# Optimization experiments

Hardware: AMD Instinct MI355X
Metric: run time of the kernel (lower is better)

Reference implementation:

```python
import jax, jax.numpy as jnp
import numpy as np

OVERLAP_THRESHOLD = 0.5
NEG_POS_RATIO = 3
ALPHA = 1.0


def cxcy_to_xy(cxcy):
    return jnp.concatenate([cxcy[..., :2] - cxcy[..., 2:] / 2,
                            cxcy[..., :2] + cxcy[..., 2:] / 2], axis=-1)


def xy_to_cxcy(xy):
    return jnp.concatenate([(xy[..., :2] + xy[..., 2:]) / 2,
                            xy[..., 2:] - xy[..., :2]], axis=-1)


def cxcy_to_gcxgcy(cxcy, priors_cxcy):
    return jnp.concatenate([
        (cxcy[..., :2] - priors_cxcy[..., :2]) / (priors_cxcy[..., 2:] / 10.0),
        jnp.log(cxcy[..., 2:] / priors_cxcy[..., 2:]) * 5.0], axis=-1)


def jaccard(a, b):
    # a: [N,4] xy, b: [P,4] xy -> [N,P]
    lo = jnp.maximum(a[:, None, :2], b[None, :, :2])
    hi = jnp.minimum(a[:, None, 2:], b[None, :, 2:])
    inter = jnp.prod(jnp.clip(hi - lo, 0.0), axis=-1)  # [N,P]
    area_a = jnp.prod(a[:, 2:] - a[:, :2], axis=-1)  # [N]
    area_b = jnp.prod(b[:, 2:] - b[:, :2], axis=-1)  # [P]
    return inter / (area_a[:, None] + area_b[None, :] - inter)


def _match_one(boxes_i, labels_i, priors_cxcy, priors_xy):
    n_objects = boxes_i.shape[0]
    overlap = jaccard(boxes_i, priors_xy)  # [N,P]
    overlap_for_each_prior = overlap.max(axis=0)  # [P]
    object_for_each_prior = overlap.argmax(axis=0)  # [P]
    prior_for_each_object = overlap.argmax(axis=1)  # [N]
    # force each object to own its best prior
    object_for_each_prior = object_for_each_prior.at[prior_for_each_object].set(
        jnp.arange(n_objects))
    overlap_for_each_prior = overlap_for_each_prior.at[prior_for_each_object].set(1.0)
    labels_for_each_prior = labels_i[object_for_each_prior]
    labels_for_each_prior = jnp.where(overlap_for_each_prior < OVERLAP_THRESHOLD,
                                      0, labels_for_each_prior)
    matched = boxes_i[object_for_each_prior]  # [P,4]
    true_locs = cxcy_to_gcxgcy(xy_to_cxcy(matched), priors_cxcy)  # [P,4]
    return true_locs, labels_for_each_prior


def reference(predicted_locs, predicted_scores, boxes, labels, priors_cxcy):
    B, P, C = predicted_scores.shape
    priors_xy = cxcy_to_xy(priors_cxcy)
    true_locs, true_classes = jax.vmap(
        _match_one, in_axes=(0, 0, None, None))(boxes, labels, priors_cxcy, priors_xy)
    # true_locs: [B,P,4], true_classes: [B,P]
    positive = true_classes != 0  # [B,P]
    n_pos = positive.sum(axis=1)  # [B]
    n_pos_total = n_pos.sum()

    # SmoothL1 (beta=1, mean over selected elements = n_pos_total*4)
    d = predicted_locs - true_locs
    ad = jnp.abs(d)
    sl1 = jnp.where(ad < 1.0, 0.5 * d * d, ad - 0.5)  # [B,P,4]
    loc_loss = (sl1 * positive[..., None]).sum() / (n_pos_total.astype(jnp.float32) * 4.0)

    # per-prior cross-entropy
    logp = jax.nn.log_softmax(predicted_scores, axis=-1)  # [B,P,C]
    conf_all = -jnp.take_along_axis(logp, true_classes[..., None], axis=-1)[..., 0]  # [B,P]

    conf_pos_sum = jnp.where(positive, conf_all, 0.0).sum()
    conf_neg = jnp.where(positive, 0.0, conf_all)
    conf_neg_sorted = jnp.sort(conf_neg, axis=1)[:, ::-1]  # descending
    n_hard_neg = NEG_POS_RATIO * n_pos  # [B]
    rank = jnp.arange(P)[None, :]
    hard_neg_mask = rank < n_hard_neg[:, None]
    conf_hard_neg_sum = jnp.where(hard_neg_mask, conf_neg_sorted, 0.0).sum()

    conf_loss = (conf_hard_neg_sum + conf_pos_sum) / n_pos_total.astype(jnp.float32)
    return conf_loss + ALPHA * loc_loss


def setup_inputs() -> dict:
    key = jax.random.key(0)
    ks = jax.random.split(key, 7)
    B, P, C, N = 128, 8732, 21, 16
    predicted_locs = jax.random.normal(ks[0], (B, P, 4), dtype=jnp.float32)
    predicted_scores = jax.random.normal(ks[1], (B, P, C), dtype=jnp.float32)
    # valid xy boxes in [0,1]
    p1 = jax.random.uniform(ks[2], (B, N, 2)) * 0.85
    wh = jax.random.uniform(ks[3], (B, N, 2), minval=0.02, maxval=0.15)
    boxes = jnp.concatenate([p1, jnp.minimum(p1 + wh, 1.0)], axis=-1)
    labels = jax.random.randint(ks[4], (B, N), 1, C)
    cxcy = jax.random.uniform(ks[5], (P, 2))
    pwh = jax.random.uniform(ks[6], (P, 2), minval=0.05, maxval=0.5)
    priors_cxcy = jnp.concatenate([cxcy, pwh], axis=-1)
    return {"predicted_locs": predicted_locs, "predicted_scores": predicted_scores,
            "boxes": boxes, "labels": labels, "priors_cxcy": priors_cxcy}
```

## Files before the change

kernel.cpp:

```cpp
#include <hip/hip_runtime.h>


#define MAXN 16

__device__ __forceinline__ float sl1f(float d) {
    float ad = fabsf(d);
    return ad < 1.0f ? 0.5f * d * d : ad - 0.5f;
}

__global__ __launch_bounds__(256) void k_bestprior(
    const float* __restrict__ boxes,
    const float* __restrict__ priors,
    int P, int N,
    int* __restrict__ pfo,
    int* __restrict__ npos)
{
    __shared__ float rv[4];
    __shared__ int   riq[4];
    const int id = blockIdx.x;
    const int tid = threadIdx.x;
    const int lane = tid & 63, wid = tid >> 6;

    if (tid == 0 && (id % N) == 0) npos[id / N] = 0;

    const float* bp = boxes + (size_t)id * 4;
    const float bx1 = bp[0], by1 = bp[1], bx2 = bp[2], by2 = bp[3];
    const float ba = (bx2 - bx1) * (by2 - by1);

    float v = -1.0f; int i = 0x7fffffff;
    for (int p = tid; p < P; p += 256) {
        float4 pr = ((const float4*)priors)[p];
        float px1 = pr.x - pr.z * 0.5f, py1 = pr.y - pr.w * 0.5f;
        float px2 = pr.x + pr.z * 0.5f, py2 = pr.y + pr.w * 0.5f;
        float parea = (px2 - px1) * (py2 - py1);
        float iw = fmaxf(fminf(bx2, px2) - fmaxf(bx1, px1), 0.0f);
        float ih = fmaxf(fminf(by2, py2) - fmaxf(by1, py1), 0.0f);
        float inter = iw * ih;
        float iou = inter / (ba + parea - inter);
        if (iou > v) { v = iou; i = p; }
    }
#pragma unroll
    for (int off = 32; off > 0; off >>= 1) {
        float ov = __shfl_down(v, off);
        int   oi = __shfl_down(i, off);
        if (ov > v || (ov == v && oi < i)) { v = ov; i = oi; }
    }
    if (lane == 0) { rv[wid] = v; riq[wid] = i; }
    __syncthreads();
    if (tid == 0) {
        for (int w = 1; w < 4; w++) {
            float ov = rv[w]; int oi = riq[w];
            if (ov > v || (ov == v && oi < i)) { v = ov; i = oi; }
        }
        pfo[id] = i;
    }
}

__global__ __launch_bounds__(256) void k_assign(
    const float* __restrict__ plocs,
    const float* __restrict__ boxes,
    const int*   __restrict__ labels,
    const float* __restrict__ priors,
    const int*   __restrict__ pfo,
    int P, int N, int nchunk,
    int*   __restrict__ cls_out,
    int*   __restrict__ npos,
    float* __restrict__ locpart)
{
    __shared__ float sx1[MAXN], sy1[MAXN], sx2[MAXN], sy2[MAXN], barea[MAXN];
    __shared__ int   blab[MAXN], spfo[MAXN];
    __shared__ float redf[4];
    __shared__ int   redi[4];

    const int b = blockIdx.y;
    const int tid = threadIdx.x;
    const int lane = tid & 63, wid = tid >> 6;
    if (N > MAXN) N = MAXN;

    if (tid < N) {
        const float* bp = boxes + ((size_t)b * N + tid) * 4;
        float x1 = bp[0], y1 = bp[1], x2 = bp[2], y2 = bp[3];
        sx1[tid] = x1; sy1[tid] = y1; sx2[tid] = x2; sy2[tid] = y2;
        barea[tid] = (x2 - x1) * (y2 - y1);
        blab[tid] = labels[(size_t)b * N + tid];
        spfo[tid] = pfo[b * N + tid];
    }
    __syncthreads();

    const int p = blockIdx.x * 256 + tid;
    float locs = 0.0f; int np = 0;
    if (p < P) {
        float4 pr = ((const float4*)priors)[p];
        float px1 = pr.x - pr.z * 0.5f, py1 = pr.y - pr.w * 0.5f;
        float px2 = pr.x + pr.z * 0.5f, py2 = pr.y + pr.w * 0.5f;
        float parea = (px2 - px1) * (py2 - py1);
        float best = -1.0f; int bestn = 0;
#pragma unroll
        for (int n = 0; n < MAXN; n++) {
            if (n < N) {
                float iw = fmaxf(fminf(sx2[n], px2) - fmaxf(sx1[n], px1), 0.0f);
                float ih = fmaxf(fminf(sy2[n], py2) - fmaxf(sy1[n], py1), 0.0f);
                float inter = iw * ih;
                float iou = inter / (barea[n] + parea - inter);
                if (iou > best) { best = iou; bestn = n; }
            }
        }
#pragma unroll
        for (int n = 0; n < MAXN; n++) {
            if (n < N && spfo[n] == p) { bestn = n; best = 1.0f; }
        }
        int lab = (best < 0.5f) ? 0 : blab[bestn];
        cls_out[(size_t)b * P + p] = lab;
        if (lab != 0) {
            np = 1;
            int n = bestn;
            float cx = (sx1[n] + sx2[n]) * 0.5f, cy = (sy1[n] + sy2[n]) * 0.5f;
            float w = sx2[n] - sx1[n], h = sy2[n] - sy1[n];
            float g0 = (cx - pr.x) / (pr.z / 10.0f);
            float g1 = (cy - pr.y) / (pr.w / 10.0f);
            float g2 = logf(w / pr.z) * 5.0f;
            float g3 = logf(h / pr.w) * 5.0f;
            float4 pl = ((const float4*)plocs)[(size_t)b * P + p];
            locs = sl1f(pl.x - g0) + sl1f(pl.y - g1) + sl1f(pl.z - g2) + sl1f(pl.w - g3);
        }
    }
#pragma unroll
    for (int off = 32; off > 0; off >>= 1) {
        locs += __shfl_down(locs, off);
        np   += __shfl_down(np, off);
    }
    if (lane == 0) { redf[wid] = locs; redi[wid] = np; }
    __syncthreads();
    if (tid == 0) {
        float L = redf[0] + redf[1] + redf[2] + redf[3];
        int   c = redi[0] + redi[1] + redi[2] + redi[3];
        if (c) atomicAdd(&npos[b], c);
        locpart[b * nchunk + blockIdx.x] = L;
    }
}

__global__ __launch_bounds__(256) void k_conf(
    const float* __restrict__ scores,
    int total, int C,
    float* __restrict__ slot,
    float* __restrict__ possum)
{
    extern __shared__ float sh[];
    __shared__ float redf[4];
    const int tid = threadIdx.x;
    const int lane = tid & 63, wid = tid >> 6;
    const int blk = blockIdx.x;
    const int row0 = blk * 256;

    const size_t f4base = (size_t)row0 * C / 4;
    const size_t f4total = (size_t)total * C / 4;
    const int f4blk = 64 * C;
    const float4* __restrict__ s4 = (const float4*)scores;
    for (int j = tid; j < f4blk; j += 256) {
        size_t g = f4base + j;
        if (g < f4total) ((float4*)sh)[j] = s4[g];
    }
    __syncthreads();

    const int idx = row0 + tid;
    float posc = 0.0f;
    if (idx < total) {
        int lab = ((const int*)slot)[idx];
        const float* r = sh + tid * C;
        float m = -3.402823466e38f;
        for (int c = 0; c < C; c++) m = fmaxf(m, r[c]);
        float sum = 0.0f;
        for (int c = 0; c < C; c++) sum += __expf(r[c] - m);
        float conf = m + __logf(sum) - r[lab];
        if (lab != 0) { posc = conf; conf = 0.0f; }
        slot[idx] = conf;
    }
#pragma unroll
    for (int off = 32; off > 0; off >>= 1) posc += __shfl_down(posc, off);
    if (lane == 0) redf[wid] = posc;
    __syncthreads();
    if (tid == 0) possum[blk] = redf[0] + redf[1] + redf[2] + redf[3];
}

__global__ __launch_bounds__(1024) void k_hard(
    const float* __restrict__ conf,
    const int* __restrict__ npos,
    int P,
    float* __restrict__ hardsum)
{
    extern __shared__ unsigned int u[];
    __shared__ int   redi[16 * 3];
    __shared__ float redf2[16];
    __shared__ int   redi2[16];
    const int b = blockIdx.x, tid = threadIdx.x;
    const int lane = tid & 63, wid = tid >> 6;
    const int nthr = blockDim.x, nw = nthr >> 6;
    long long kk = (long long)npos[b] * 3;
    int k = kk > P ? P : (int)kk;
    if (k <= 0) {
        if (tid == 0) hardsum[b] = 0.0f;
        return;
    }

    for (int p = tid; p < P; p += nthr) u[p] = __float_as_uint(conf[(size_t)b * P + p]);
    __syncthreads();

    unsigned lo = 0u, hi = 0x7F800000u;
    while (lo < hi) {
        unsigned span = hi - lo;
        if (span >= 8) {
            unsigned q = span >> 2;
            unsigned m1 = lo + q, m2 = lo + 2 * q, m3 = lo + 3 * q;
            int c1 = 0, c2 = 0, c3 = 0;
            for (int p = tid; p < P; p += nthr) {
                unsigned v = u[p];
                c1 += (int)__popcll(__ballot(v >= m1));
                c2 += (int)__popcll(__ballot(v >= m2));
                c3 += (int)__popcll(__ballot(v >= m3));
            }
            if (lane == 0) {
                redi[wid * 3 + 0] = c1; redi[wid * 3 + 1] = c2; redi[wid * 3 + 2] = c3;
            }
            __syncthreads();
            int C1 = 0, C2 = 0, C3 = 0;
            for (int w = 0; w < nw; w++) {
                C1 += redi[w * 3 + 0]; C2 += redi[w * 3 + 1]; C3 += redi[w * 3 + 2];
            }
            __syncthreads();
            if      (C3 >= k) lo = m3;
            else if (C2 >= k) { lo = m2; hi = m3 - 1; }
            else if (C1 >= k) { lo = m1; hi = m2 - 1; }
            else              hi = m1 - 1;
        } else {
            unsigned mid = lo + ((span + 1) >> 1);
            int c = 0;
            for (int p = tid; p < P; p += nthr)
                c += (int)__popcll(__ballot(u[p] >= mid));
            if (lane == 0) redi[wid * 3] = c;
            __syncthreads();
            int Cc = 0;
            for (int w = 0; w < nw; w++) Cc += redi[w * 3];
            __syncthreads();
            if (Cc >= k) lo = mid; else hi = mid - 1;
        }
    }

    float t = __uint_as_float(lo);
    float sgt = 0.0f; int cgt = 0;
    for (int p = tid; p < P; p += nthr) {
        float v = __uint_as_float(u[p]);
        if (v > t) { sgt += v; cgt++; }
    }
#pragma unroll
    for (int off = 32; off > 0; off >>= 1) {
        sgt += __shfl_down(sgt, off);
        cgt += __shfl_down(cgt, off);
    }
    if (lane == 0) { redf2[wid] = sgt; redi2[wid] = cgt; }
    __syncthreads();
    if (tid == 0) {
        float S = 0.0f; int Cg = 0;
        for (int w = 0; w < nw; w++) { S += redf2[w]; Cg += redi2[w]; }
        hardsum[b] = S + (float)(k - Cg) * t;
    }
}

__global__ __launch_bounds__(1024) void k_final(
    const int* __restrict__ npos, const float* __restrict__ locpart,
    const float* __restrict__ hardsum, const float* __restrict__ possum,
    int B, int nloc, int nconf, float* __restrict__ out)
{
    const int tid = threadIdx.x, lane = tid & 63, wid = tid >> 6;
    __shared__ float rf[3 * 16];
    __shared__ int   ri[16];
    float lp = 0, pp = 0, hp = 0; int np = 0;
    for (int i = tid; i < B; i += 1024) { np += npos[i]; hp += hardsum[i]; }
    for (int i = tid; i < nloc; i += 1024) lp += locpart[i];
    for (int i = tid; i < nconf; i += 1024) pp += possum[i];
#pragma unroll
    for (int off = 32; off > 0; off >>= 1) {
        np += __shfl_down(np, off); lp += __shfl_down(lp, off);
        pp += __shfl_down(pp, off); hp += __shfl_down(hp, off);
    }
    if (lane == 0) { ri[wid] = np; rf[wid] = lp; rf[16 + wid] = pp; rf[32 + wid] = hp; }
    __syncthreads();
    if (tid == 0) {
        int nw = (int)(blockDim.x >> 6);
        float L = 0, Pp = 0, H = 0; int Np = 0;
        for (int w = 0; w < nw; w++) { Np += ri[w]; L += rf[w]; Pp += rf[16 + w]; H += rf[32 + w]; }
        float npf = (float)Np;
        out[0] = (H + Pp) / npf + L / (npf * 4.0f);
    }
}

extern "C" void kernel_launch(void* const* d_in, const int* in_sizes, int n_in,
                              void* d_out, int out_size, void* d_ws, size_t ws_size,
                              hipStream_t stream)
{
    const float* plocs  = (const float*)d_in[0];
    const float* scores = (const float*)d_in[1];
    const float* boxes  = (const float*)d_in[2];
    const int*   labels = (const int*)d_in[3];
    const float* priors = (const float*)d_in[4];

    int P = in_sizes[4] / 4;
    int B = in_sizes[0] / (P * 4);
    int C = in_sizes[1] / (in_sizes[0] / 4);
    int N = in_sizes[3] / B;
    int total = B * P;
    int nconf = (total + 255) / 256;
    int nchunk = (P + 255) / 256;
    int BN = B * N;

    char* w = (char*)d_ws;
    float* slot    = (float*)w;  w += (size_t)total * sizeof(float);
    int*   npos    = (int*)w;    w += (size_t)B * sizeof(int);
    int*   pfo     = (int*)w;    w += (size_t)BN * sizeof(int);
    float* locpart = (float*)w;  w += (size_t)B * nchunk * sizeof(float);
    float* hardsum = (float*)w;  w += (size_t)B * sizeof(float);
    float* possum  = (float*)w;

    k_bestprior<<<BN, 256, 0, stream>>>(boxes, priors, P, N, pfo, npos);

    dim3 ga(nchunk, B);
    k_assign<<<ga, 256, 0, stream>>>(plocs, boxes, labels, priors, pfo,
                                     P, N, nchunk, (int*)slot, npos, locpart);

    size_t sm2 = (size_t)256 * C * sizeof(float);
    k_conf<<<nconf, 256, sm2, stream>>>(scores, total, C, slot, possum);

    k_hard<<<B, 1024, (size_t)P * sizeof(unsigned int), stream>>>(slot, npos, P, hardsum);

    k_final<<<1, 1024, 0, stream>>>(npos, locpart, hardsum, possum,
                                    B, B * nchunk, nconf, (float*)d_out);
}
```

Measured before the change: 238.7 us.

## Fuse conf loss into assign kernel and keep hard-neg values in registers

Merges the softmax cross-entropy computation into the prior-assignment kernel, so the label array is no longer written to and re-read from global memory and one launch goes away. The hard-negative selection kernel now holds each thread's conf values in a fixed register array instead of shared memory, and gains an occupancy hint in its launch bounds. It also adds an unroll pragma to the best-prior loop. The fused kernel needs per-row shared memory for scores, and the register array assumes P fits within 16×1024 elements.

```diff
diff --git a/kernel.cpp b/kernel.cpp
--- a/kernel.cpp
+++ b/kernel.cpp
@@ -2,6 +2,7 @@
 
 
 #define MAXN 16
+#define MAXE 16
 
 __device__ __forceinline__ float sl1f(float d) {
     float ad = fabsf(d);
@@ -28,6 +29,7 @@
     const float ba = (bx2 - bx1) * (by2 - by1);
 
     float v = -1.0f; int i = 0x7fffffff;
+#pragma unroll 2
     for (int p = tid; p < P; p += 256) {
         float4 pr = ((const float4*)priors)[p];
         float px1 = pr.x - pr.z * 0.5f, py1 = pr.y - pr.w * 0.5f;
@@ -56,26 +58,31 @@
     }
 }
 
-__global__ __launch_bounds__(256) void k_assign(
+__global__ __launch_bounds__(256) void k_fused(
     const float* __restrict__ plocs,
+    const float* __restrict__ scores,
     const float* __restrict__ boxes,
     const int*   __restrict__ labels,
     const float* __restrict__ priors,
     const int*   __restrict__ pfo,
-    int P, int N, int nchunk,
-    int*   __restrict__ cls_out,
+    int P, int C, int N, int nchunk,
+    float* __restrict__ conf_out,
     int*   __restrict__ npos,
-    float* __restrict__ locpart)
-{
+    float* __restrict__ locpart,
+    float* __restrict__ pospart)
+{
+    extern __shared__ float sh[];
     __shared__ float sx1[MAXN], sy1[MAXN], sx2[MAXN], sy2[MAXN], barea[MAXN];
     __shared__ int   blab[MAXN], spfo[MAXN];
-    __shared__ float redf[4];
+    __shared__ float redf[4], redp[4];
     __shared__ int   redi[4];
 
     const int b = blockIdx.y;
     const int tid = threadIdx.x;
     const int lane = tid & 63, wid = tid >> 6;
     if (N > MAXN) N = MAXN;
+    const int p0 = blockIdx.x * 256;
+    const int rows = min(256, P - p0);
 
     if (tid < N) {
         const float* bp = boxes + ((size_t)b * N + tid) * 4;
@@ -85,10 +92,19 @@
         blab[tid] = labels[(size_t)b * N + tid];
         spfo[tid] = pfo[b * N + tid];
     }
-    __syncthreads();
-
-    const int p = blockIdx.x * 256 + tid;
-    float locs = 0.0f; int np = 0;
+
+    {
+        const size_t f4base = ((size_t)b * P + p0) * C / 4;
+        const int f4cnt = (rows * C + 3) / 4;
+        const float4* __restrict__ s4 = (const float4*)scores;
+        for (int j = tid; j < f4cnt; j += 256)
+            ((float4*)sh)[j] = s4[f4base + j];
+    }
+    __syncthreads();
+
+    const int p = p0 + tid;
+    float locs = 0.0f, posc = 0.0f, conf = 0.0f;
+    int np = 0;
     if (p < P) {
         float4 pr = ((const float4*)priors)[p];
         float px1 = pr.x - pr.z * 0.5f, py1 = pr.y - pr.w * 0.5f;
@@ -109,10 +125,17 @@
         for (int n = 0; n < MAXN; n++) {
             if (n < N && spfo[n] == p) { bestn = n; best = 1.0f; }
         }
-        int lab = (best < 0.5f) ? 0 : blab[bestn];
-        cls_out[(size_t)b * P + p] = lab;
+        const int lab = (best < 0.5f) ? 0 : blab[bestn];
+
+        const float* r = sh + tid * C;
+        float m = -3.402823466e38f;
+        for (int c = 0; c < C; c++) m = fmaxf(m, r[c]);
+        float sum = 0.0f;
+        for (int c = 0; c < C; c++) sum += __expf(r[c] - m);
+        float ce = m + __logf(sum) - r[lab];
+
         if (lab != 0) {
-            np = 1;
+            posc = ce; np = 1;
             int n = bestn;
             float cx = (sx1[n] + sx2[n]) * 0.5f, cy = (sy1[n] + sy2[n]) * 0.5f;
             float w = sx2[n] - sx1[n], h = sy2[n] - sy1[n];
@@ -122,79 +145,42 @@
             float g3 = logf(h / pr.w) * 5.0f;
             float4 pl = ((const float4*)plocs)[(size_t)b * P + p];
             locs = sl1f(pl.x - g0) + sl1f(pl.y - g1) + sl1f(pl.z - g2) + sl1f(pl.w - g3);
-        }
+        } else {
+            conf = ce;
+        }
+        conf_out[(size_t)b * P + p] = conf;
     }
 #pragma unroll
     for (int off = 32; off > 0; off >>= 1) {
         locs += __shfl_down(locs, off);
+        posc += __shfl_down(posc, off);
         np   += __shfl_down(np, off);
     }
-    if (lane == 0) { redf[wid] = locs; redi[wid] = np; }
+    if (lane == 0) { redf[wid] = locs; redp[wid] = posc; redi[wid] = np; }
     __syncthreads();
     if (tid == 0) {
         float L = redf[0] + redf[1] + redf[2] + redf[3];
+        float Pp = redp[0] + redp[1] + redp[2] + redp[3];
         int   c = redi[0] + redi[1] + redi[2] + redi[3];
         if (c) atomicAdd(&npos[b], c);
         locpart[b * nchunk + blockIdx.x] = L;
-    }
-}
-
-__global__ __launch_bounds__(256) void k_conf(
-    const float* __restrict__ scores,
-    int total, int C,
-    float* __restrict__ slot,
-    float* __restrict__ possum)
-{
-    extern __shared__ float sh[];
-    __shared__ float redf[4];
-    const int tid = threadIdx.x;
-    const int lane = tid & 63, wid = tid >> 6;
-    const int blk = blockIdx.x;
-    const int row0 = blk * 256;
-
-    const size_t f4base = (size_t)row0 * C / 4;
-    const size_t f4total = (size_t)total * C / 4;
-    const int f4blk = 64 * C;
-    const float4* __restrict__ s4 = (const float4*)scores;
-    for (int j = tid; j < f4blk; j += 256) {
-        size_t g = f4base + j;
-        if (g < f4total) ((float4*)sh)[j] = s4[g];
-    }
-    __syncthreads();
-
-    const int idx = row0 + tid;
-    float posc = 0.0f;
-    if (idx < total) {
-        int lab = ((const int*)slot)[idx];
-        const float* r = sh + tid * C;
-        float m = -3.402823466e38f;
-        for (int c = 0; c < C; c++) m = fmaxf(m, r[c]);
-        float sum = 0.0f;
-        for (int c = 0; c < C; c++) sum += __expf(r[c] - m);
-        float conf = m + __logf(sum) - r[lab];
-        if (lab != 0) { posc = conf; conf = 0.0f; }
-        slot[idx] = conf;
-    }
-#pragma unroll
-    for (int off = 32; off > 0; off >>= 1) posc += __shfl_down(posc, off);
-    if (lane == 0) redf[wid] = posc;
-    __syncthreads();
-    if (tid == 0) possum[blk] = redf[0] + redf[1] + redf[2] + redf[3];
-}
-
-__global__ __launch_bounds__(1024) void k_hard(
+        pospart[b * nchunk + blockIdx.x] = Pp;
+    }
+}
+
+__global__ __launch_bounds__(1024, 4) void k_hard(
     const float* __restrict__ conf,
     const int* __restrict__ npos,
     int P,
     float* __restrict__ hardsum)
 {
-    extern __shared__ unsigned int u[];
     __shared__ int   redi[16 * 3];
     __shared__ float redf2[16];
     __shared__ int   redi2[16];
     const int b = blockIdx.x, tid = threadIdx.x;
     const int lane = tid & 63, wid = tid >> 6;
     const int nthr = blockDim.x, nw = nthr >> 6;
+    const int ne = (P + nthr - 1) / nthr;
     long long kk = (long long)npos[b] * 3;
     int k = kk > P ? P : (int)kk;
     if (k <= 0) {
@@ -202,8 +188,12 @@
         return;
     }
 
-    for (int p = tid; p < P; p += nthr) u[p] = __float_as_uint(conf[(size_t)b * P + p]);
-    __syncthreads();
+    unsigned e[MAXE];
+#pragma unroll
+    for (int j = 0; j < MAXE; j++) {
+        int p = j * nthr + tid;
+        e[j] = (j < ne && p < P) ? __float_as_uint(conf[(size_t)b * P + p]) : 0u;
+    }
 
     unsigned lo = 0u, hi = 0x7F800000u;
     while (lo < hi) {
@@ -212,11 +202,14 @@
             unsigned q = span >> 2;
             unsigned m1 = lo + q, m2 = lo + 2 * q, m3 = lo + 3 * q;
             int c1 = 0, c2 = 0, c3 = 0;
-            for (int p = tid; p < P; p += nthr) {
-                unsigned v = u[p];
-                c1 += (int)__popcll(__ballot(v >= m1));
-                c2 += (int)__popcll(__ballot(v >= m2));
-                c3 += (int)__popcll(__ballot(v >= m3));
+#pragma unroll
+            for (int j = 0; j < MAXE; j++) {
+                if (j < ne) {
+                    unsigned v = e[j];
+                    c1 += (int)__popcll(__ballot(v >= m1));
+                    c2 += (int)__popcll(__ballot(v >= m2));
+                    c3 += (int)__popcll(__ballot(v >= m3));
+                }
             }
             if (lane == 0) {
                 redi[wid * 3 + 0] = c1; redi[wid * 3 + 1] = c2; redi[wid * 3 + 2] = c3;
@@ -234,8 +227,9 @@
         } else {
             unsigned mid = lo + ((span + 1) >> 1);
             int c = 0;
-            for (int p = tid; p < P; p += nthr)
-                c += (int)__popcll(__ballot(u[p] >= mid));
+#pragma unroll
+            for (int j = 0; j < MAXE; j++)
+                if (j < ne) c += (int)__popcll(__ballot(e[j] >= mid));
             if (lane == 0) redi[wid * 3] = c;
             __syncthreads();
             int Cc = 0;
@@ -247,9 +241,12 @@
 
     float t = __uint_as_float(lo);
     float sgt = 0.0f; int cgt = 0;
-    for (int p = tid; p < P; p += nthr) {
-        float v = __uint_as_float(u[p]);
-        if (v > t) { sgt += v; cgt++; }
+#pragma unroll
+    for (int j = 0; j < MAXE; j++) {
+        if (j < ne) {
+            float v = __uint_as_float(e[j]);
+            if (v > t) { sgt += v; cgt++; }
+        }
     }
 #pragma unroll
     for (int off = 32; off > 0; off >>= 1) {
@@ -267,16 +264,15 @@
 
 __global__ __launch_bounds__(1024) void k_final(
     const int* __restrict__ npos, const float* __restrict__ locpart,
-    const float* __restrict__ hardsum, const float* __restrict__ possum,
-    int B, int nloc, int nconf, float* __restrict__ out)
+    const float* __restrict__ pospart, const float* __restrict__ hardsum,
+    int B, int nloc, float* __restrict__ out)
 {
     const int tid = threadIdx.x, lane = tid & 63, wid = tid >> 6;
     __shared__ float rf[3 * 16];
     __shared__ int   ri[16];
     float lp = 0, pp = 0, hp = 0; int np = 0;
     for (int i = tid; i < B; i += 1024) { np += npos[i]; hp += hardsum[i]; }
-    for (int i = tid; i < nloc; i += 1024) lp += locpart[i];
-    for (int i = tid; i < nconf; i += 1024) pp += possum[i];
+    for (int i = tid; i < nloc; i += 1024) { lp += locpart[i]; pp += pospart[i]; }
 #pragma unroll
     for (int off = 32; off > 0; off >>= 1) {
         np += __shfl_down(np, off); lp += __shfl_down(lp, off);
@@ -307,30 +303,26 @@
     int B = in_sizes[0] / (P * 4);
     int C = in_sizes[1] / (in_sizes[0] / 4);
     int N = in_sizes[3] / B;
-    int total = B * P;
-    int nconf = (total + 255) / 256;
     int nchunk = (P + 255) / 256;
     int BN = B * N;
 
     char* w = (char*)d_ws;
-    float* slot    = (float*)w;  w += (size_t)total * sizeof(float);
+    float* slot    = (float*)w;  w += (size_t)B * P * sizeof(float);
     int*   npos    = (int*)w;    w += (size_t)B * sizeof(int);
     int*   pfo     = (int*)w;    w += (size_t)BN * sizeof(int);
     float* locpart = (float*)w;  w += (size_t)B * nchunk * sizeof(float);
-    float* hardsum = (float*)w;  w += (size_t)B * sizeof(float);
-    float* possum  = (float*)w;
+    float* pospart = (float*)w;  w += (size_t)B * nchunk * sizeof(float);
+    float* hardsum = (float*)w;
 
     k_bestprior<<<BN, 256, 0, stream>>>(boxes, priors, P, N, pfo, npos);
 
     dim3 ga(nchunk, B);
-    k_assign<<<ga, 256, 0, stream>>>(plocs, boxes, labels, priors, pfo,
-                                     P, N, nchunk, (int*)slot, npos, locpart);
-
-    size_t sm2 = (size_t)256 * C * sizeof(float);
-    k_conf<<<nconf, 256, sm2, stream>>>(scores, total, C, slot, possum);
-
-    k_hard<<<B, 1024, (size_t)P * sizeof(unsigned int), stream>>>(slot, npos, P, hardsum);
-
-    k_final<<<1, 1024, 0, stream>>>(npos, locpart, hardsum, possum,
-                                    B, B * nchunk, nconf, (float*)d_out);
-}
+    size_t smf = (size_t)256 * C * sizeof(float);
+    k_fused<<<ga, 256, smf, stream>>>(plocs, scores, boxes, labels, priors, pfo,
+                                      P, C, N, nchunk, slot, npos, locpart, pospart);
+
+    k_hard<<<B, 1024, 0, stream>>>(slot, npos, P, hardsum);
+
+    k_final<<<1, 1024, 0, stream>>>(npos, locpart, pospart, hardsum,
+                                    B, B * nchunk, (float*)d_out);
+}
```

New measurement: 221.4 us. -7.3%, faster.
